# Kernel tuning notes

Hardware: AMD Instinct MI355X
Metric: run time of the kernel (lower is better)

## Reference

```python
import jax, jax.numpy as jnp
import numpy as np

K = 16

def _local_cov(points):
    # points: [B, N, 3]. FoldingNet-style local covariance feature.
    xx = jnp.sum(points * points, axis=-1)                       # [B,N]
    inner = jnp.einsum('bnd,bmd->bnm', points, points)           # [B,N,N]
    pd = -xx[:, :, None] + 2.0 * inner - xx[:, None, :]          # negative sq dist
    _, idx = jax.lax.top_k(pd, K)                                # [B,N,K] nearest first (self at 0)
    n0 = jnp.take_along_axis(points, idx[:, :, 0][:, :, None], axis=1)  # [B,N,3]
    n1 = jnp.take_along_axis(points, idx[:, :, 1][:, :, None], axis=1)  # [B,N,3]
    cov = n0[..., :, None] * n1[..., None, :]                    # [B,N,3,3] outer product
    B, N = points.shape[0], points.shape[1]
    return jnp.concatenate([points, cov.reshape(B, N, 9)], axis=-1)     # [B,N,12]

def _stage(x, w1, b1, wr, br, w2, b2):
    h = jax.nn.relu(x @ w1 + b1)
    h = jax.nn.relu(h + (h @ wr + br))   # ResidualLinearLayer then ReLU
    return h @ w2 + b2                   # [B,N,1]

def setup_inputs() -> dict:
    key = jax.random.key(0)
    ks = jax.random.split(key, 16)
    B, N, F = 8, 4096, 512
    s = 0.02
    d = {
        'latent': jax.random.normal(ks[0], (B, N, F), jnp.float32),
        'reconstructed_points': jax.random.normal(ks[1], (B, 3, N), jnp.float32),
        's1_w1': jax.random.normal(ks[2], (F + 12, F), jnp.float32) * s,
        's1_b1': jnp.zeros((F,), jnp.float32),
        's1_wr': jax.random.normal(ks[3], (F, F), jnp.float32) * s,
        's1_br': jnp.zeros((F,), jnp.float32),
        's1_w2': jax.random.normal(ks[4], (F, 1), jnp.float32) * s,
        's1_b2': jnp.zeros((1,), jnp.float32),
        's2_w1': jax.random.normal(ks[5], (F + 1, F), jnp.float32) * s,
        's2_b1': jnp.zeros((F,), jnp.float32),
        's2_wr': jax.random.normal(ks[6], (F, F), jnp.float32) * s,
        's2_br': jnp.zeros((F,), jnp.float32),
        's2_w2': jax.random.normal(ks[7], (F, 1), jnp.float32) * s,
        's2_b2': jnp.zeros((1,), jnp.float32),
        's3_w1': jax.random.normal(ks[8], (F + 1, F), jnp.float32) * s,
        's3_b1': jnp.zeros((F,), jnp.float32),
        's3_wr': jax.random.normal(ks[9], (F, F), jnp.float32) * s,
        's3_br': jnp.zeros((F,), jnp.float32),
        's3_w2': jax.random.normal(ks[10], (F, 1), jnp.float32) * s,
        's3_b2': jnp.zeros((1,), jnp.float32),
    }
    return d

def reference(latent, reconstructed_points,
              s1_w1, s1_b1, s1_wr, s1_br, s1_w2, s1_b2,
              s2_w1, s2_b1, s2_wr, s2_br, s2_w2, s2_b2,
              s3_w1, s3_b1, s3_wr, s3_br, s3_w2, s3_b2):
    pts = jnp.transpose(reconstructed_points, (0, 2, 1))   # [B,N,3]
    local = _local_cov(pts)                                 # [B,N,12]
    f1 = jnp.concatenate([latent, local], axis=-1)
    std1 = _stage(f1, s1_w1, s1_b1, s1_wr, s1_br, s1_w2, s1_b2)
    f2 = jnp.concatenate([latent, std1], axis=-1)
    std2 = std1 + _stage(f2, s2_w1, s2_b1, s2_wr, s2_br, s2_w2, s2_b2)
    f3 = jnp.concatenate([latent, std2], axis=-1)
    std3 = std2 + _stage(f3, s3_w1, s3_b1, s3_wr, s3_br, s3_w2, s3_b2)
    return std3   # [B,N,1]
```

## Files before the change

### kernel.cpp

```cpp
#include <hip/hip_runtime.h>

typedef __bf16 bf16x8 __attribute__((ext_vector_type(8)));
typedef float f32x16 __attribute__((ext_vector_type(16)));

__device__ __forceinline__ unsigned short f2bf(float f) {
  unsigned u = __float_as_uint(f);
  u += 0x7FFFu + ((u >> 16) & 1u);
  return (unsigned short)(u >> 16);
}

__device__ __forceinline__ void gload_lds16(const void* g, void* l) {
  __builtin_amdgcn_global_load_lds((const __attribute__((address_space(1))) void*)g,
                                   (__attribute__((address_space(3))) void*)l,
                                   16, 0, 0);
}

#define NPTS 4096
#define LDX 576

__global__ __launch_bounds__(256) void convw6_kernel(
    const float* w0, const float* w1, const float* w2,
    const float* r0, const float* r1, const float* r2,
    unsigned short* d0, unsigned short* d1, unsigned short* d2,
    unsigned short* e0, unsigned short* e1, unsigned short* e2) {
  int z = blockIdx.z;
  const float* src; unsigned short* dst; int Ksrc, Kpad, addI;
  switch (z) {
    case 0: src = w0; dst = d0; Ksrc = 524; Kpad = 576; addI = 0; break;
    case 1: src = w1; dst = d1; Ksrc = 513; Kpad = 576; addI = 0; break;
    case 2: src = w2; dst = d2; Ksrc = 513; Kpad = 576; addI = 0; break;
    case 3: src = r0; dst = e0; Ksrc = 512; Kpad = 512; addI = 1; break;
    case 4: src = r1; dst = e1; Ksrc = 512; Kpad = 512; addI = 1; break;
    default: src = r2; dst = e2; Ksrc = 512; Kpad = 512; addI = 1; break;
  }
  int k0 = blockIdx.x * 32;
  if (k0 >= Kpad) return;
  __shared__ float tile[32][33];
  int n0 = blockIdx.y * 32;
  int tx = threadIdx.x & 31, ty = threadIdx.x >> 5;
#pragma unroll
  for (int r = 0; r < 32; r += 8) {
    int k = k0 + ty + r, n = n0 + tx;
    tile[ty + r][tx] = (k < Ksrc) ? src[(size_t)k * 512 + n] : 0.f;
  }
  __syncthreads();
#pragma unroll
  for (int r = 0; r < 32; r += 8) {
    int n = n0 + ty + r, k = k0 + tx;
    float v = tile[tx][ty + r];
    if (addI && n == k) v += 1.0f;
    dst[(size_t)n * Kpad + k] = f2bf(v);
  }
}

__global__ __launch_bounds__(256) void conv_latent_kernel(const float* __restrict__ latent,
                                                          unsigned short* __restrict__ X) {
  size_t idx = (size_t)blockIdx.x * 256 + threadIdx.x;
  size_t m = idx >> 7;
  int c4 = (int)(idx & 127) * 4;
  float4 v = *(const float4*)(latent + m * 512 + c4);
  ushort4 o;
  o.x = f2bf(v.x); o.y = f2bf(v.y); o.z = f2bf(v.z); o.w = f2bf(v.w);
  *(ushort4*)(X + m * LDX + c4) = o;
}

__device__ __forceinline__ void merge1(float& v, int& j, int mk) {
  float ov = __shfl_xor(v, mk); int oj = __shfl_xor(j, mk);
  bool take = (ov > v) || (ov == v && oj < j);
  v = take ? ov : v; j = take ? oj : j;
}

__global__ __launch_bounds__(512) void knn_kernel(const float* __restrict__ rp,
                                                  unsigned short* __restrict__ X) {
  __shared__ float4 P[NPTS];
  int b = blockIdx.y;
  const float* base = rp + (size_t)b * 3 * NPTS;
  for (int j = threadIdx.x; j < NPTS; j += 512) {
    float x = base[j], y = base[NPTS + j], z = base[2 * NPTS + j];
    float xx = __fadd_rn(__fadd_rn(__fmul_rn(x, x), __fmul_rn(y, y)), __fmul_rn(z, z));
    P[j] = make_float4(x, y, z, -xx);
  }
  __syncthreads();
  int wave = threadIdx.x >> 6, lane = threadIdx.x & 63;
  int grp = lane >> 4, slice = lane & 15;
  int il0 = wave * 8 + grp * 2;
  int ia = blockIdx.x * 64 + il0;
  int ib = ia + 1;
  float4 pa = P[ia], pb = P[ib];
  float ax = 2.f * pa.x, ay = 2.f * pa.y, az = 2.f * pa.z;
  float bx = 2.f * pb.x, by = 2.f * pb.y, bz = 2.f * pb.z;
  float va = -3.4e38f, vb = -3.4e38f;
  int ta = 0, tb = 0;
  int sta = ((ia & 15) == slice) ? (ia >> 4) : -1;
  int stb = ((ib & 15) == slice) ? (ib >> 4) : -1;
  const float4* pp = P + slice;
#pragma unroll 8
  for (int t = 0; t < NPTS / 16; ++t) {
    float4 pj = pp[t * 16];
    float ea = __builtin_fmaf(ax, pj.x, __builtin_fmaf(ay, pj.y,
               __builtin_fmaf(az, pj.z, pj.w)));
    float eb = __builtin_fmaf(bx, pj.x, __builtin_fmaf(by, pj.y,
               __builtin_fmaf(bz, pj.z, pj.w)));
    ea = (t == sta) ? -3.4e38f : ea;
    eb = (t == stb) ? -3.4e38f : eb;
    bool ca = ea > va; va = ca ? ea : va; ta = ca ? t : ta;
    bool cb = eb > vb; vb = cb ? eb : vb; tb = cb ? t : tb;
  }
  int ja = ta * 16 + slice, jb = tb * 16 + slice;
#pragma unroll
  for (int mk = 1; mk <= 8; mk <<= 1) {
    merge1(va, ja, mk);
    merge1(vb, jb, mk);
  }
  if (slice == 0) {
#pragma unroll
    for (int p = 0; p < 2; ++p) {
      float4 pi = (p == 0) ? pa : pb;
      float4 p1 = P[(p == 0) ? ja : jb];
      size_t row = (size_t)b * NPTS + ia + p;
      unsigned short* xp = X + row * LDX + 512;
      float vals[12] = { pi.x, pi.y, pi.z,
                         pi.x * p1.x, pi.x * p1.y, pi.x * p1.z,
                         pi.y * p1.x, pi.y * p1.y, pi.y * p1.z,
                         pi.z * p1.x, pi.z * p1.y, pi.z * p1.z };
#pragma unroll
      for (int k = 0; k < 12; ++k) xp[k] = f2bf(vals[k]);
#pragma unroll
      for (int k = 12; k < 32; ++k) xp[k] = 0;
    }
  }
}

#define BM 256
#define BN 128
#define BK 64
#define GRP 520
#define MBLK 128

__global__ __launch_bounds__(512) void gemm_relu_kernel(
    const unsigned short* __restrict__ Xb, const unsigned short* __restrict__ Wt,
    const float* __restrict__ bias, unsigned short* __restrict__ H,
    int K, int ldx, int ldw,
    const float* __restrict__ stdv, const float* __restrict__ w1row) {
  __shared__ unsigned short As[32 * GRP];
  __shared__ unsigned short Bs[16 * GRP];
  const int t = threadIdx.x;
  const int wave = t >> 6, lane = t & 63;
  const int flat = blockIdx.y * gridDim.x + blockIdx.x;
  const int m0 = (flat & (MBLK - 1)) * BM;
  const int n0 = (flat >> 7) * BN;
  const int wm = (wave >> 1) * 64, wn = (wave & 1) * 64;
  const int srow = lane >> 3;
  const int sslot = (lane & 7) ^ srow;
  const int l31 = lane & 31, hi = lane >> 5;
  const int w7 = l31 & 7, g2 = l31 >> 3;
  f32x16 acc[2][2] = {};
  for (int kt = 0; kt < K; kt += BK) {
#pragma unroll
    for (int r = 0; r < 4; ++r) {
      int ga = wave + r * 8;
      gload_lds16(Xb + (size_t)(m0 + ga * 8 + srow) * ldx + kt + sslot * 8, As + ga * GRP);
    }
#pragma unroll
    for (int r = 0; r < 2; ++r) {
      int gb = wave + r * 8;
      gload_lds16(Wt + (size_t)(n0 + gb * 8 + srow) * ldw + kt + sslot * 8, Bs + gb * GRP);
    }
    __syncthreads();
#pragma unroll
    for (int ks = 0; ks < 4; ++ks) {
      int qx = (ks * 2 + hi) ^ w7;
      bf16x8 a[2], bb[2];
#pragma unroll
      for (int i = 0; i < 2; ++i)
        a[i] = *(const bf16x8*)(As + ((wm >> 3) + i * 4 + g2) * GRP + w7 * 64 + qx * 8);
#pragma unroll
      for (int j = 0; j < 2; ++j)
        bb[j] = *(const bf16x8*)(Bs + ((wn >> 3) + j * 4 + g2) * GRP + w7 * 64 + qx * 8);
#pragma unroll
      for (int i = 0; i < 2; ++i)
#pragma unroll
        for (int j = 0; j < 2; ++j)
          acc[i][j] = __builtin_amdgcn_mfma_f32_32x32x16_bf16(a[i], bb[j], acc[i][j], 0, 0, 0);
    }
    __syncthreads();
  }
  if (w1row) {
    float wv[2];
#pragma unroll
    for (int j = 0; j < 2; ++j) wv[j] = w1row[n0 + wn + j * 32 + l31];
#pragma unroll
    for (int i = 0; i < 2; ++i) {
#pragma unroll
      for (int rg = 0; rg < 16; ++rg) {
        int row = m0 + wm + i * 32 + (rg & 3) + 8 * (rg >> 2) + 4 * hi;
        float sv = stdv[row];
        acc[i][0][rg] += sv * wv[0];
        acc[i][1][rg] += sv * wv[1];
      }
    }
  }
#pragma unroll
  for (int j = 0; j < 2; ++j) {
    int col = n0 + wn + j * 32 + l31;
    float bv = bias[col];
#pragma unroll
    for (int i = 0; i < 2; ++i) {
#pragma unroll
      for (int rg = 0; rg < 16; ++rg) {
        int row = m0 + wm + i * 32 + (rg & 3) + 8 * (rg >> 2) + 4 * hi;
        float v = acc[i][j][rg] + bv;
        v = v > 0.f ? v : 0.f;
        H[(size_t)row * 512 + col] = f2bf(v);
      }
    }
  }
}

__global__ __launch_bounds__(512) void gemm_res_kernel(
    const unsigned short* __restrict__ H1, const unsigned short* __restrict__ Wt,
    const float* __restrict__ br, const float* __restrict__ w2,
    float* __restrict__ so) {
  __shared__ unsigned short As[32 * GRP];
  __shared__ unsigned short Bs[16 * GRP];
  const int t = threadIdx.x;
  const int wave = t >> 6, lane = t & 63;
  const int flat = blockIdx.y * gridDim.x + blockIdx.x;
  const int m0 = (flat & (MBLK - 1)) * BM;
  const int n0 = (flat >> 7) * BN;
  const int wm = (wave >> 1) * 64, wn = (wave & 1) * 64;
  const int srow = lane >> 3;
  const int sslot = (lane & 7) ^ srow;
  const int l31 = lane & 31, hi = lane >> 5;
  const int w7 = l31 & 7, g2 = l31 >> 3;
  f32x16 acc[2][2] = {};
  for (int kt = 0; kt < 512; kt += BK) {
#pragma unroll
    for (int r = 0; r < 4; ++r) {
      int ga = wave + r * 8;
      gload_lds16(H1 + (size_t)(m0 + ga * 8 + srow) * 512 + kt + sslot * 8, As + ga * GRP);
    }
#pragma unroll
    for (int r = 0; r < 2; ++r) {
      int gb = wave + r * 8;
      gload_lds16(Wt + (size_t)(n0 + gb * 8 + srow) * 512 + kt + sslot * 8, Bs + gb * GRP);
    }
    __syncthreads();
#pragma unroll
    for (int ks = 0; ks < 4; ++ks) {
      int qx = (ks * 2 + hi) ^ w7;
      bf16x8 a[2], bb[2];
#pragma unroll
      for (int i = 0; i < 2; ++i)
        a[i] = *(const bf16x8*)(As + ((wm >> 3) + i * 4 + g2) * GRP + w7 * 64 + qx * 8);
#pragma unroll
      for (int j = 0; j < 2; ++j)
        bb[j] = *(const bf16x8*)(Bs + ((wn >> 3) + j * 4 + g2) * GRP + w7 * 64 + qx * 8);
#pragma unroll
      for (int i = 0; i < 2; ++i)
#pragma unroll
        for (int j = 0; j < 2; ++j)
          acc[i][j] = __builtin_amdgcn_mfma_f32_32x32x16_bf16(a[i], bb[j], acc[i][j], 0, 0, 0);
    }
    __syncthreads();
  }
  float pr[2][16];
#pragma unroll
  for (int i = 0; i < 2; ++i)
#pragma unroll
    for (int rg = 0; rg < 16; ++rg) pr[i][rg] = 0.f;
#pragma unroll
  for (int j = 0; j < 2; ++j) {
    int col = n0 + wn + j * 32 + l31;
    float bv = br[col], wv = w2[col];
#pragma unroll
    for (int i = 0; i < 2; ++i)
#pragma unroll
      for (int rg = 0; rg < 16; ++rg) {
        float v = acc[i][j][rg] + bv;
        v = v > 0.f ? v : 0.f;
        pr[i][rg] += v * wv;
      }
  }
#pragma unroll
  for (int i = 0; i < 2; ++i)
#pragma unroll
    for (int rg = 0; rg < 16; ++rg) {
      float s = pr[i][rg];
      s += __shfl_xor(s, 1); s += __shfl_xor(s, 2); s += __shfl_xor(s, 4);
      s += __shfl_xor(s, 8); s += __shfl_xor(s, 16);
      if (l31 == 0) {
        int row = m0 + wm + i * 32 + (rg & 3) + 8 * (rg >> 2) + 4 * hi;
        atomicAdd(&so[row], s);
      }
    }
}

__global__ __launch_bounds__(256) void init_so_kernel(float* so, const float* b2) {
  int m = blockIdx.x * 256 + threadIdx.x;
  so[m] = b2[0];
}
__global__ __launch_bounds__(256) void update_kernel(float* std_cum, float* so,
                                                     const float* b2_next, int first) {
  int m = blockIdx.x * 256 + threadIdx.x;
  float s = so[m];
  if (!first) s += std_cum[m];
  std_cum[m] = s;
  so[m] = b2_next[0];
}
__global__ __launch_bounds__(256) void finalize_kernel(float* out, const float* std_cum,
                                                       const float* so) {
  int m = blockIdx.x * 256 + threadIdx.x;
  out[m] = std_cum[m] + so[m];
}

extern "C" void kernel_launch(void* const* d_in, const int* in_sizes, int n_in,
                              void* d_out, int out_size, void* d_ws, size_t ws_size,
                              hipStream_t stream) {
  const int B = 8, N = NPTS, M = B * N;
  const float* latent = (const float*)d_in[0];
  const float* rp = (const float*)d_in[1];
  const float* w1[3] = {(const float*)d_in[2], (const float*)d_in[8], (const float*)d_in[14]};
  const float* b1[3] = {(const float*)d_in[3], (const float*)d_in[9], (const float*)d_in[15]};
  const float* wr[3] = {(const float*)d_in[4], (const float*)d_in[10], (const float*)d_in[16]};
  const float* br[3] = {(const float*)d_in[5], (const float*)d_in[11], (const float*)d_in[17]};
  const float* w2[3] = {(const float*)d_in[6], (const float*)d_in[12], (const float*)d_in[18]};
  const float* b2[3] = {(const float*)d_in[7], (const float*)d_in[13], (const float*)d_in[19]};

  char* ws = (char*)d_ws;
  auto carve = [&](size_t bytes) {
    char* p = ws;
    ws += (bytes + 255) & ~(size_t)255;
    return p;
  };
  unsigned short* X  = (unsigned short*)carve((size_t)M * LDX * 2);
  unsigned short* H1 = (unsigned short*)carve((size_t)M * 512 * 2);
  unsigned short* W1t[3], *Wrt[3];
  for (int s = 0; s < 3; ++s) W1t[s] = (unsigned short*)carve((size_t)512 * LDX * 2);
  for (int s = 0; s < 3; ++s) Wrt[s] = (unsigned short*)carve((size_t)512 * 512 * 2);
  float* std_cum = (float*)carve((size_t)M * 4);
  float* so      = (float*)carve((size_t)M * 4);

  convw6_kernel<<<dim3(LDX / 32, 16, 6), 256, 0, stream>>>(
      w1[0], w1[1], w1[2], wr[0], wr[1], wr[2],
      W1t[0], W1t[1], W1t[2], Wrt[0], Wrt[1], Wrt[2]);
  conv_latent_kernel<<<(M * 128) / 256, 256, 0, stream>>>(latent, X);
  knn_kernel<<<dim3(N / 64, B), 512, 0, stream>>>(rp, X);
  init_so_kernel<<<M / 256, 256, 0, stream>>>(so, b2[0]);

  for (int s = 0; s < 3; ++s) {
    if (s == 0) {
      gemm_relu_kernel<<<dim3(512 / BN, M / BM), 512, 0, stream>>>(
          X, W1t[s], b1[s], H1, LDX, LDX, LDX, nullptr, nullptr);
    } else {
      gemm_relu_kernel<<<dim3(512 / BN, M / BM), 512, 0, stream>>>(
          X, W1t[s], b1[s], H1, 512, LDX, LDX, std_cum, w1[s] + (size_t)512 * 512);
    }
    gemm_res_kernel<<<dim3(4, M / BM), 512, 0, stream>>>(H1, Wrt[s], br[s], w2[s], so);
    if (s < 2)
      update_kernel<<<M / 256, 256, 0, stream>>>(std_cum, so, b2[s + 1], s == 0 ? 1 : 0);
  }
  finalize_kernel<<<M / 256, 256, 0, stream>>>((float*)d_out, std_cum, so);
}
```

Measured before the change: 342.8 us.

## Double-buffer LDS tiles and widen GEMM N-tile to 256

Both GEMM kernels now use a 256x256 block tile, with each wave computing 64x128, and a double-buffered dynamic LDS staging scheme. The next K-tile's global-to-LDS loads are issued before the current tile is computed, using explicit vmcnt waits and raw barriers. This is meant to overlap memory latency with MFMA work and halve the number of B-tile reloads per row block. In exchange it roughly doubles LDS use per block (about 133KB) and raises register pressure from the larger accumulators. The grid also shrinks to 2x128 blocks, which may leave CUs underused.

```diff
diff --git a/kernel.cpp b/kernel.cpp
--- a/kernel.cpp
+++ b/kernel.cpp
@@ -132,76 +132,96 @@
 }
 
 #define BM 256
-#define BN 128
+#define BN 256
 #define BK 64
 #define GRP 520
 #define MBLK 128
+#define LDSU16 (2 * 64 * GRP)
 
 __global__ __launch_bounds__(512) void gemm_relu_kernel(
     const unsigned short* __restrict__ Xb, const unsigned short* __restrict__ Wt,
     const float* __restrict__ bias, unsigned short* __restrict__ H,
     int K, int ldx, int ldw,
     const float* __restrict__ stdv, const float* __restrict__ w1row) {
-  __shared__ unsigned short As[32 * GRP];
-  __shared__ unsigned short Bs[16 * GRP];
+  extern __shared__ unsigned short S[];
   const int t = threadIdx.x;
   const int wave = t >> 6, lane = t & 63;
   const int flat = blockIdx.y * gridDim.x + blockIdx.x;
   const int m0 = (flat & (MBLK - 1)) * BM;
   const int n0 = (flat >> 7) * BN;
-  const int wm = (wave >> 1) * 64, wn = (wave & 1) * 64;
+  const int wm = (wave >> 1) * 64;
+  const int wn = (wave & 1) * 128;
   const int srow = lane >> 3;
   const int sslot = (lane & 7) ^ srow;
   const int l31 = lane & 31, hi = lane >> 5;
   const int w7 = l31 & 7, g2 = l31 >> 3;
-  f32x16 acc[2][2] = {};
-  for (int kt = 0; kt < K; kt += BK) {
+  const unsigned short* Arow = Xb + (size_t)(m0 + srow) * ldx + sslot * 8;
+  const unsigned short* Brow = Wt + (size_t)(n0 + srow) * ldw + sslot * 8;
+  f32x16 acc[2][4] = {};
+  const int nt = K / BK;
+  auto STAGE = [&](int buf, int kt) {
 #pragma unroll
     for (int r = 0; r < 4; ++r) {
-      int ga = wave + r * 8;
-      gload_lds16(Xb + (size_t)(m0 + ga * 8 + srow) * ldx + kt + sslot * 8, As + ga * GRP);
-    }
-#pragma unroll
-    for (int r = 0; r < 2; ++r) {
-      int gb = wave + r * 8;
-      gload_lds16(Wt + (size_t)(n0 + gb * 8 + srow) * ldw + kt + sslot * 8, Bs + gb * GRP);
-    }
-    __syncthreads();
+      int g = wave + r * 8;
+      gload_lds16(Arow + (size_t)g * 8 * ldx + kt, S + buf * (64 * GRP) + g * GRP);
+    }
+#pragma unroll
+    for (int r = 0; r < 4; ++r) {
+      int g = wave + r * 8;
+      gload_lds16(Brow + (size_t)g * 8 * ldw + kt, S + buf * (64 * GRP) + (32 + g) * GRP);
+    }
+  };
+  STAGE(0, 0);
+  for (int tt = 0; tt < nt; ++tt) {
+    const int cur = tt & 1;
+    if (tt + 1 < nt) {
+      STAGE(cur ^ 1, (tt + 1) * BK);
+      asm volatile("s_waitcnt vmcnt(8)" ::: "memory");
+    } else {
+      asm volatile("s_waitcnt vmcnt(0)" ::: "memory");
+    }
+    __builtin_amdgcn_s_barrier();
+    asm volatile("" ::: "memory");
+    const unsigned short* Sa = S + cur * (64 * GRP);
+    const unsigned short* Sb = Sa + 32 * GRP;
 #pragma unroll
     for (int ks = 0; ks < 4; ++ks) {
       int qx = (ks * 2 + hi) ^ w7;
-      bf16x8 a[2], bb[2];
+      bf16x8 a[2], bb[4];
 #pragma unroll
       for (int i = 0; i < 2; ++i)
-        a[i] = *(const bf16x8*)(As + ((wm >> 3) + i * 4 + g2) * GRP + w7 * 64 + qx * 8);
-#pragma unroll
-      for (int j = 0; j < 2; ++j)
-        bb[j] = *(const bf16x8*)(Bs + ((wn >> 3) + j * 4 + g2) * GRP + w7 * 64 + qx * 8);
+        a[i] = *(const bf16x8*)(Sa + ((wm >> 3) + i * 4 + g2) * GRP + w7 * 64 + qx * 8);
+#pragma unroll
+      for (int j = 0; j < 4; ++j)
+        bb[j] = *(const bf16x8*)(Sb + ((wn >> 3) + j * 4 + g2) * GRP + w7 * 64 + qx * 8);
 #pragma unroll
       for (int i = 0; i < 2; ++i)
 #pragma unroll
-        for (int j = 0; j < 2; ++j)
+        for (int j = 0; j < 4; ++j)
           acc[i][j] = __builtin_amdgcn_mfma_f32_32x32x16_bf16(a[i], bb[j], acc[i][j], 0, 0, 0);
     }
-    __syncthreads();
+    asm volatile("" ::: "memory");
+    __builtin_amdgcn_sched_barrier(0);
+    __builtin_amdgcn_s_barrier();
+    asm volatile("" ::: "memory");
   }
   if (w1row) {
-    float wv[2];
-#pragma unroll
-    for (int j = 0; j < 2; ++j) wv[j] = w1row[n0 + wn + j * 32 + l31];
+    float wv[4];
+#pragma unroll
+    for (int j = 0; j < 4; ++j) wv[j] = w1row[n0 + wn + j * 32 + l31];
 #pragma unroll
     for (int i = 0; i < 2; ++i) {
 #pragma unroll
       for (int rg = 0; rg < 16; ++rg) {
         int row = m0 + wm + i * 32 + (rg & 3) + 8 * (rg >> 2) + 4 * hi;
         float sv = stdv[row];
-        acc[i][0][rg] += sv * wv[0];
-        acc[i][1][rg] += sv * wv[1];
+#pragma unroll
+        for (int j = 0; j < 4; ++j) acc[i][j][rg] += sv * wv[j];
       }
     }
   }
 #pragma unroll
-  for (int j = 0; j < 2; ++j) {
+  for (int j = 0; j < 4; ++j) {
     int col = n0 + wn + j * 32 + l31;
     float bv = bias[col];
 #pragma unroll
@@ -221,72 +241,85 @@
     const unsigned short* __restrict__ H1, const unsigned short* __restrict__ Wt,
     const float* __restrict__ br, const float* __restrict__ w2,
     float* __restrict__ so) {
-  __shared__ unsigned short As[32 * GRP];
-  __shared__ unsigned short Bs[16 * GRP];
+  extern __shared__ unsigned short S[];
   const int t = threadIdx.x;
   const int wave = t >> 6, lane = t & 63;
   const int flat = blockIdx.y * gridDim.x + blockIdx.x;
   const int m0 = (flat & (MBLK - 1)) * BM;
   const int n0 = (flat >> 7) * BN;
-  const int wm = (wave >> 1) * 64, wn = (wave & 1) * 64;
+  const int wm = (wave >> 1) * 64;
+  const int wn = (wave & 1) * 128;
   const int srow = lane >> 3;
   const int sslot = (lane & 7) ^ srow;
   const int l31 = lane & 31, hi = lane >> 5;
   const int w7 = l31 & 7, g2 = l31 >> 3;
-  f32x16 acc[2][2] = {};
-  for (int kt = 0; kt < 512; kt += BK) {
+  const unsigned short* Arow = H1 + (size_t)(m0 + srow) * 512 + sslot * 8;
+  const unsigned short* Brow = Wt + (size_t)(n0 + srow) * 512 + sslot * 8;
+  f32x16 acc[2][4] = {};
+  auto STAGE = [&](int buf, int kt) {
 #pragma unroll
     for (int r = 0; r < 4; ++r) {
-      int ga = wave + r * 8;
-      gload_lds16(H1 + (size_t)(m0 + ga * 8 + srow) * 512 + kt + sslot * 8, As + ga * GRP);
-    }
-#pragma unroll
-    for (int r = 0; r < 2; ++r) {
-      int gb = wave + r * 8;
-      gload_lds16(Wt + (size_t)(n0 + gb * 8 + srow) * 512 + kt + sslot * 8, Bs + gb * GRP);
-    }
-    __syncthreads();
+      int g = wave + r * 8;
+      gload_lds16(Arow + (size_t)g * 8 * 512 + kt, S + buf * (64 * GRP) + g * GRP);
+    }
+#pragma unroll
+    for (int r = 0; r < 4; ++r) {
+      int g = wave + r * 8;
+      gload_lds16(Brow + (size_t)g * 8 * 512 + kt, S + buf * (64 * GRP) + (32 + g) * GRP);
+    }
+  };
+  STAGE(0, 0);
+  const int nt = 512 / BK;
+  for (int tt = 0; tt < nt; ++tt) {
+    const int cur = tt & 1;
+    if (tt + 1 < nt) {
+      STAGE(cur ^ 1, (tt + 1) * BK);
+      asm volatile("s_waitcnt vmcnt(8)" ::: "memory");
+    } else {
+      asm volatile("s_waitcnt vmcnt(0)" ::: "memory");
+    }
+    __builtin_amdgcn_s_barrier();
+    asm volatile("" ::: "memory");
+    const unsigned short* Sa = S + cur * (64 * GRP);
+    const unsigned short* Sb = Sa + 32 * GRP;
 #pragma unroll
     for (int ks = 0; ks < 4; ++ks) {
       int qx = (ks * 2 + hi) ^ w7;
-      bf16x8 a[2], bb[2];
+      bf16x8 a[2], bb[4];
 #pragma unroll
       for (int i = 0; i < 2; ++i)
-        a[i] = *(const bf16x8*)(As + ((wm >> 3) + i * 4 + g2) * GRP + w7 * 64 + qx * 8);
-#pragma unroll
-      for (int j = 0; j < 2; ++j)
-        bb[j] = *(const bf16x8*)(Bs + ((wn >> 3) + j * 4 + g2) * GRP + w7 * 64 + qx * 8);
+        a[i] = *(const bf16x8*)(Sa + ((wm >> 3) + i * 4 + g2) * GRP + w7 * 64 + qx * 8);
+#pragma unroll
+      for (int j = 0; j < 4; ++j)
+        bb[j] = *(const bf16x8*)(Sb + ((wn >> 3) + j * 4 + g2) * GRP + w7 * 64 + qx * 8);
 #pragma unroll
       for (int i = 0; i < 2; ++i)
 #pragma unroll
-        for (int j = 0; j < 2; ++j)
+        for (int j = 0; j < 4; ++j)
           acc[i][j] = __builtin_amdgcn_mfma_f32_32x32x16_bf16(a[i], bb[j], acc[i][j], 0, 0, 0);
     }
-    __syncthreads();
-  }
-  float pr[2][16];
-#pragma unroll
-  for (int i = 0; i < 2; ++i)
-#pragma unroll
-    for (int rg = 0; rg < 16; ++rg) pr[i][rg] = 0.f;
-#pragma unroll
-  for (int j = 0; j < 2; ++j) {
+    asm volatile("" ::: "memory");
+    __builtin_amdgcn_sched_barrier(0);
+    __builtin_amdgcn_s_barrier();
+    asm volatile("" ::: "memory");
+  }
+  float bv[4], wv[4];
+#pragma unroll
+  for (int j = 0; j < 4; ++j) {
     int col = n0 + wn + j * 32 + l31;
-    float bv = br[col], wv = w2[col];
-#pragma unroll
-    for (int i = 0; i < 2; ++i)
-#pragma unroll
-      for (int rg = 0; rg < 16; ++rg) {
-        float v = acc[i][j][rg] + bv;
+    bv[j] = br[col]; wv[j] = w2[col];
+  }
+#pragma unroll
+  for (int i = 0; i < 2; ++i) {
+#pragma unroll
+    for (int rg = 0; rg < 16; ++rg) {
+      float s = 0.f;
+#pragma unroll
+      for (int j = 0; j < 4; ++j) {
+        float v = acc[i][j][rg] + bv[j];
         v = v > 0.f ? v : 0.f;
-        pr[i][rg] += v * wv;
+        s += v * wv[j];
       }
-  }
-#pragma unroll
-  for (int i = 0; i < 2; ++i)
-#pragma unroll
-    for (int rg = 0; rg < 16; ++rg) {
-      float s = pr[i][rg];
       s += __shfl_xor(s, 1); s += __shfl_xor(s, 2); s += __shfl_xor(s, 4);
       s += __shfl_xor(s, 8); s += __shfl_xor(s, 16);
       if (l31 == 0) {
@@ -294,6 +327,7 @@
         atomicAdd(&so[row], s);
       }
     }
+  }
 }
 
 __global__ __launch_bounds__(256) void init_so_kernel(float* so, const float* b2) {
@@ -341,6 +375,8 @@
   float* std_cum = (float*)carve((size_t)M * 4);
   float* so      = (float*)carve((size_t)M * 4);
 
+  const size_t ldsBytes = (size_t)LDSU16 * 2;
+
   convw6_kernel<<<dim3(LDX / 32, 16, 6), 256, 0, stream>>>(
       w1[0], w1[1], w1[2], wr[0], wr[1], wr[2],
       W1t[0], W1t[1], W1t[2], Wrt[0], Wrt[1], Wrt[2]);
@@ -350,13 +386,14 @@
 
   for (int s = 0; s < 3; ++s) {
     if (s == 0) {
-      gemm_relu_kernel<<<dim3(512 / BN, M / BM), 512, 0, stream>>>(
+      gemm_relu_kernel<<<dim3(512 / BN, M / BM), 512, ldsBytes, stream>>>(
           X, W1t[s], b1[s], H1, LDX, LDX, LDX, nullptr, nullptr);
     } else {
-      gemm_relu_kernel<<<dim3(512 / BN, M / BM), 512, 0, stream>>>(
+      gemm_relu_kernel<<<dim3(512 / BN, M / BM), 512, ldsBytes, stream>>>(
           X, W1t[s], b1[s], H1, 512, LDX, LDX, std_cum, w1[s] + (size_t)512 * 512);
     }
-    gemm_res_kernel<<<dim3(4, M / BM), 512, 0, stream>>>(H1, Wrt[s], br[s], w2[s], so);
+    gemm_res_kernel<<<dim3(512 / BN, M / BM), 512, ldsBytes, stream>>>(
+        H1, Wrt[s], br[s], w2[s], so);
     if (s < 2)
       update_kernel<<<M / 256, 256, 0, stream>>>(std_cum, so, b2[s + 1], s == 0 ? 1 : 0);
   }
```

After: 330.7 us. -3.6%, faster.
